# Kernel optimization log

Measured on AMD Instinct MI355X. Metric: run time of the kernel, lower is better.

## Reference

```python
import jax, jax.numpy as jnp
import numpy as np

D_MODEL = 1024
N_HEADS = 16
D_FF = 4096
EPS = 1e-5


def _layer_norm(x, scale, bias):
    mu = jnp.mean(x, axis=-1, keepdims=True)
    var = jnp.mean(jnp.square(x - mu), axis=-1, keepdims=True)
    return (x - mu) * jax.lax.rsqrt(var + EPS) * scale + bias


def setup_inputs() -> dict:
    key = jax.random.key(0)
    ks = jax.random.split(key, 12)
    B, L, D, F = 8, 1024, D_MODEL, D_FF
    s = 0.02
    inp = {
        "x": jax.random.normal(ks[0], (B, L, D), dtype=jnp.float32),
        "mask": jax.random.randint(ks[1], (B, L, L), 0, 2).astype(bool),
        "Wq": jax.random.normal(ks[2], (D, D), dtype=jnp.float32) * s,
        "bq": jnp.zeros((D,), jnp.float32),
        "Wk": jax.random.normal(ks[3], (D, D), dtype=jnp.float32) * s,
        "bk": jnp.zeros((D,), jnp.float32),
        "Wv": jax.random.normal(ks[4], (D, D), dtype=jnp.float32) * s,
        "bv": jnp.zeros((D,), jnp.float32),
        "Wo": jax.random.normal(ks[5], (D, D), dtype=jnp.float32) * s,
        "bo": jnp.zeros((D,), jnp.float32),
        "ln1_s": jnp.ones((D,), jnp.float32),
        "ln1_b": jnp.zeros((D,), jnp.float32),
        "ln2_s": jnp.ones((D,), jnp.float32),
        "ln2_b": jnp.zeros((D,), jnp.float32),
        "W1": jax.random.normal(ks[6], (F, D), dtype=jnp.float32) * s,
        "b1": jnp.zeros((F,), jnp.float32),
        "W2": jax.random.normal(ks[7], (D, F), dtype=jnp.float32) * s,
        "b2": jnp.zeros((D,), jnp.float32),
    }
    return inp


def _block(x, mask, Wq, bq, Wk, bk, Wv, bv, Wo, bo,
           ln1_s, ln1_b, ln2_s, ln2_b, W1, b1, W2, b2):
    B, L, D = x.shape
    H = N_HEADS
    dk = D // H
    xn = _layer_norm(x, ln1_s, ln1_b)
    # torch Linear: y = x @ W.T + b
    Q = (xn @ Wq.T + bq).reshape(B, L, H, dk).transpose(0, 2, 1, 3)  # [B,H,L,dk]
    K = (xn @ Wk.T + bk).reshape(B, L, H, dk).transpose(0, 2, 1, 3)
    V = (xn @ Wv.T + bv).reshape(B, L, H, dk).transpose(0, 2, 1, 3)
    scores = jnp.einsum('bhqd,bhkd->bhqk', Q, K) / jnp.sqrt(jnp.float32(dk))
    m = mask[:, None, :, :]                                    # [B,1,Lq,Lk]
    scores = jnp.where(m, -jnp.inf, scores)
    fully_masked = jnp.all(m, axis=-1, keepdims=True)          # [B,1,Lq,1]
    scores = jnp.where(fully_masked, 0.0, scores)
    attn = jax.nn.softmax(scores, axis=-1)
    attn = jnp.where(fully_masked, 0.0, attn)
    out = jnp.einsum('bhqk,bhkd->bhqd', attn, V)               # [B,H,L,dk]
    out = out.transpose(0, 2, 1, 3).reshape(B, L, D)
    attn_out = out @ Wo.T + bo
    x = x + attn_out
    xn2 = _layer_norm(x, ln2_s, ln2_b)
    h = jax.nn.gelu(xn2 @ W1.T + b1, approximate=False)        # exact GELU (torch default)
    ff = h @ W2.T + b2
    return x + ff


def reference(x, mask, Wq, bq, Wk, bk, Wv, bv, Wo, bo,
              ln1_s, ln1_b, ln2_s, ln2_b, W1, b1, W2, b2):
    return _block(x, mask, Wq, bq, Wk, bk, Wv, bv, Wo, bo,
                  ln1_s, ln1_b, ln2_s, ln2_b, W1, b1, W2, b2)
```

## Files before the change

### kernel.cpp

```cpp
#include <hip/hip_runtime.h>
#include <cstdint>
#include <cstddef>

typedef __attribute__((ext_vector_type(8))) short short8;
typedef __attribute__((ext_vector_type(4))) float f32x4;
typedef __attribute__((ext_vector_type(4))) unsigned short ushort4v;

#define DEVI __device__ __forceinline__

DEVI unsigned short f2bf(float f) {
  union { float f; unsigned u; } x; x.f = f;
  unsigned r = x.u + 0x7fffu + ((x.u >> 16) & 1u);
  return (unsigned short)(r >> 16);
}

#define MFMA16(a, b, c) __builtin_amdgcn_mfma_f32_16x16x32_bf16(a, b, c, 0, 0, 0)
#define FENCE asm volatile("" ::: "memory")
#define WAITVM(n) asm volatile("s_waitcnt vmcnt(" #n ")" ::: "memory")
#define WAITLGKM0 asm volatile("s_waitcnt lgkmcnt(0)" ::: "memory")
#define BARRIER do { FENCE; __builtin_amdgcn_s_barrier(); FENCE; } while (0)

typedef __attribute__((address_space(1))) const void g_void;
typedef __attribute__((address_space(3))) void lds_void;
DEVI void gload_lds16(const void* g, void* l) {
  __builtin_amdgcn_global_load_lds((g_void*)g, (lds_void*)l, 16, 0, 0);
}

static constexpr int DM = 1024;
static constexpr int NH = 16;
static constexpr int DK = 64;
static constexpr int FF = 4096;
static constexpr int BB = 8;
static constexpr int LL = 1024;
static constexpr int TT = BB * LL;

__global__ __launch_bounds__(256) void prep_kernel(
    const float* __restrict__ Wq, const float* __restrict__ Wk,
    const float* __restrict__ Wv, const float* __restrict__ Wo,
    const float* __restrict__ W1, const float* __restrict__ W2,
    const float* __restrict__ bq, const float* __restrict__ bk,
    const float* __restrict__ bv,
    unsigned short* __restrict__ wqkv, unsigned short* __restrict__ wob,
    unsigned short* __restrict__ w1b, unsigned short* __restrict__ w2b,
    float* __restrict__ bqkv, const unsigned* __restrict__ mask,
    int* __restrict__ flag) {
  int b = blockIdx.x;
  if (b < 6144) {
    int i = b * 256 + threadIdx.x;
    const float* src; unsigned short* dst; int li;
    if (i < 131072)      { src = Wq; dst = wqkv;             li = i; }
    else if (i < 262144) { src = Wk; dst = wqkv + (1 << 20); li = i - 131072; }
    else if (i < 393216) { src = Wv; dst = wqkv + (2 << 20); li = i - 262144; }
    else if (i < 524288) { src = Wo; dst = wob;              li = i - 393216; }
    else if (i < 1048576){ src = W1; dst = w1b;              li = i - 524288; }
    else                 { src = W2; dst = w2b;              li = i - 1048576; }
    const f32x4* s4 = (const f32x4*)src;
    f32x4 a = s4[li * 2], c = s4[li * 2 + 1];
    short8 o;
    o[0] = (short)f2bf(a[0]); o[1] = (short)f2bf(a[1]);
    o[2] = (short)f2bf(a[2]); o[3] = (short)f2bf(a[3]);
    o[4] = (short)f2bf(c[0]); o[5] = (short)f2bf(c[1]);
    o[6] = (short)f2bf(c[2]); o[7] = (short)f2bf(c[3]);
    *(short8*)(dst + (size_t)li * 8) = o;
  } else if (b < 6156) {
    int i = (b - 6144) * 256 + threadIdx.x;
    bqkv[i] = (i < 1024) ? bq[i] : (i < 2048 ? bk[i - 1024] : bv[i - 2048]);
  } else {
    unsigned a = 0;
    for (int i = threadIdx.x; i < 4096; i += 256) a |= mask[i];
    #pragma unroll
    for (int off = 32; off >= 1; off >>= 1) a |= __shfl_xor(a, off);
    __shared__ unsigned sh[4];
    if ((threadIdx.x & 63) == 0) sh[threadIdx.x >> 6] = a;
    __syncthreads();
    if (threadIdx.x == 0) {
      unsigned o = sh[0] | sh[1] | sh[2] | sh[3];
      flag[0] = (o & 0xFEFEFEFEu) ? 2 : ((o & 0xFFFFFF00u) ? 1 : 0);
    }
  }
}

__global__ __launch_bounds__(256) void ln_kernel(const float* __restrict__ x,
                                                 const float* __restrict__ sc,
                                                 const float* __restrict__ bi,
                                                 unsigned short* __restrict__ out,
                                                 const void* __restrict__ mask,
                                                 unsigned* __restrict__ mp,
                                                 const int* __restrict__ flag,
                                                 int npack) {
  int row = blockIdx.x;
  int t = threadIdx.x;
  if (row >= TT) {
    int w = (row - TT) * 256 + t;
    int cls = flag[0];
    unsigned bits = 0u;
    if (cls == 1) {
      const unsigned char* mb = (const unsigned char*)mask + (size_t)w * 32;
      #pragma unroll 8
      for (int i = 0; i < 32; ++i) bits |= (mb[i] ? 1u : 0u) << i;
    } else {
      const unsigned* mi = (const unsigned*)mask + (size_t)w * 32;
      #pragma unroll 8
      for (int i = 0; i < 32; ++i) bits |= (mi[i] ? 1u : 0u) << i;
    }
    mp[w] = bits;
    return;
  }
  const f32x4* xr = (const f32x4*)(x + (size_t)row * DM);
  f32x4 v = xr[t];
  float s = v[0] + v[1] + v[2] + v[3];
  float q = v[0]*v[0] + v[1]*v[1] + v[2]*v[2] + v[3]*v[3];
  #pragma unroll
  for (int off = 32; off >= 1; off >>= 1) { s += __shfl_xor(s, off); q += __shfl_xor(q, off); }
  __shared__ float red[8];
  int wv = t >> 6;
  if ((t & 63) == 0) { red[wv] = s; red[4 + wv] = q; }
  __syncthreads();
  s = red[0] + red[1] + red[2] + red[3];
  q = red[4] + red[5] + red[6] + red[7];
  float mu = s * (1.0f / DM);
  float var = q * (1.0f / DM) - mu * mu;
  float rs = rsqrtf(var + 1e-5f);
  f32x4 sv = ((const f32x4*)sc)[t], bv = ((const f32x4*)bi)[t];
  ushort4v o;
  #pragma unroll
  for (int j = 0; j < 4; ++j) o[j] = f2bf((v[j] - mu) * rs * sv[j] + bv[j]);
  *(ushort4v*)(out + (size_t)row * DM + t * 4) = o;
}

template <int EPI>
__global__ __launch_bounds__(256, 2)
void gemm5(const unsigned short* __restrict__ A, const unsigned short* __restrict__ Bw,
           const float* __restrict__ bias, void* __restrict__ out0,
           void* __restrict__ out1, void* __restrict__ out2,
           const float* __restrict__ res, int N, int K) {
  __shared__ __align__(16) char smem[65536];
  const int t = threadIdx.x;
  const int w = t >> 6, ln = t & 63;
  const int wm = w >> 1, wn = w & 1;
  const int lg = ln >> 4, lc = ln & 15;
  const int m0 = blockIdx.x * 128, n0 = blockIdx.y * 128;
  const size_t rb = (size_t)K * 2;
  const int nk = K >> 6;

  const char* srcp[8];
  #pragma unroll
  for (int i = 0; i < 8; ++i) {
    int off = i * 4096 + t * 16;
    if (off < 16384) {
      int r = off >> 7, c = (off >> 4) & 7;
      srcp[i] = (const char*)A + (size_t)(m0 + r) * rb + ((c ^ (r & 7)) << 4);
    } else {
      int ob = off - 16384;
      int r = ob >> 7, c = (ob >> 4) & 7;
      srcp[i] = (const char*)Bw + (size_t)(n0 + r) * rb + ((c ^ (r & 7)) << 4);
    }
  }
  auto stage8 = [&](int tile) {
    char* db = smem + ((tile & 1) << 15) + t * 16;
    const size_t ko = (size_t)tile << 7;
    #pragma unroll
    for (int i = 0; i < 8; ++i) gload_lds16(srcp[i] + ko, db + i * 4096);
  };

  int aoff[4][2], boff[4][2];
  #pragma unroll
  for (int x_ = 0; x_ < 4; ++x_)
    #pragma unroll
    for (int kk = 0; kk < 2; ++kk) {
      int ra = wm * 64 + x_ * 16 + lc;
      aoff[x_][kk] = ra * 128 + (((kk * 4 + lg) ^ (ra & 7)) << 4);
      int rn = wn * 64 + x_ * 16 + lc;
      boff[x_][kk] = 16384 + rn * 128 + (((kk * 4 + lg) ^ (rn & 7)) << 4);
    }

  f32x4 acc[4][4] = {};

  stage8(0);
  for (int T = 0; T < nk; ++T) {
    if (T + 1 < nk) stage8(T + 1);
    if (T == nk - 1) { WAITVM(0); } else { WAITVM(8); }
    BARRIER;
    const char* buf = smem + ((T & 1) << 15);
    short8 afr[4][2], bfr[4][2];
    #pragma unroll
    for (int ni = 0; ni < 4; ++ni) {
      bfr[ni][0] = *(const short8*)(buf + boff[ni][0]);
      bfr[ni][1] = *(const short8*)(buf + boff[ni][1]);
    }
    #pragma unroll
    for (int mi = 0; mi < 4; ++mi) {
      afr[mi][0] = *(const short8*)(buf + aoff[mi][0]);
      afr[mi][1] = *(const short8*)(buf + aoff[mi][1]);
    }
    __builtin_amdgcn_s_setprio(1);
    #pragma unroll
    for (int mi = 0; mi < 4; ++mi)
      #pragma unroll
      for (int ni = 0; ni < 4; ++ni) {
        acc[mi][ni] = MFMA16(afr[mi][0], bfr[ni][0], acc[mi][ni]);
        acc[mi][ni] = MFMA16(afr[mi][1], bfr[ni][1], acc[mi][ni]);
      }
    __builtin_amdgcn_s_setprio(0);
    WAITLGKM0;
    BARRIER;
  }
  __syncthreads();

  const int colb = n0 + wn * 64 + lc;
  const int rowb = m0 + wm * 64 + lg * 4;
  if constexpr (EPI >= 2) {
    #pragma unroll
    for (int ni = 0; ni < 4; ++ni) {
      int col = colb + ni * 16;
      float bv = bias[col];
      #pragma unroll
      for (int mi = 0; mi < 4; ++mi)
        #pragma unroll
        for (int rr = 0; rr < 4; ++rr) {
          int row = rowb + mi * 16 + rr;
          float v = acc[mi][ni][rr] + bv;
          if constexpr (EPI == 2)
            ((float*)out0)[(size_t)row * N + col] = res[(size_t)row * N + col] + v;
          else
            ((float*)out0)[(size_t)row * N + col] += v;
        }
    }
  } else {
    short* sl = (short*)(smem + w * 9216);
    const bool isV = (EPI == 0) && (n0 + wn * 64 >= 2048);
    #pragma unroll
    for (int ni = 0; ni < 4; ++ni) {
      float bv = bias[colb + ni * 16];
      #pragma unroll
      for (int mi = 0; mi < 4; ++mi)
        #pragma unroll
        for (int rr = 0; rr < 4; ++rr) {
          int row_l = mi * 16 + lg * 4 + rr;
          int col_l = ni * 16 + lc;
          float v = acc[mi][ni][rr] + bv;
          if constexpr (EPI == 1) {
            float u2 = v * v;
            float mexp = v * (-2.302206744f - 0.102953795f * u2);
            v = v / (1.0f + exp2f(mexp));
          }
          if (isV) sl[col_l * 72 + row_l] = (short)f2bf(v);
          else     sl[row_l * 72 + col_l] = (short)f2bf(v);
        }
    }
    const int s8 = ln >> 3, c8 = ln & 7;
    if constexpr (EPI == 0) {
      const int b_ = m0 >> 10;
      const int l0 = (m0 & 1023) + wm * 64;
      const int h_ = ((n0 + wn * 64) >> 6) & 15;
      const size_t bh = (size_t)(b_ * NH + h_);
      if (n0 + wn * 64 < 2048) {
        char* dst = (char*)((n0 + wn * 64 < 1024) ? out0 : out1) + (((bh << 10) + l0) << 7);
        #pragma unroll
        for (int j = 0; j < 8; ++j) {
          short8 v8 = *(const short8*)(sl + (j * 8 + s8) * 72 + c8 * 8);
          *(short8*)(dst + j * 1024 + ln * 16) = v8;
        }
      } else {
        char* dst = (char*)out2 + bh * 131072 + l0 * 2 + c8 * 16;
        #pragma unroll
        for (int j = 0; j < 8; ++j) {
          short8 v8 = *(const short8*)(sl + (j * 8 + s8) * 72 + c8 * 8);
          *(short8*)(dst + (size_t)(j * 8 + s8) * 2048) = v8;
        }
      }
    } else {
      char* dst = (char*)out0 + (size_t)(m0 + wm * 64) * ((size_t)N * 2) +
                  (size_t)(n0 + wn * 64) * 2 + c8 * 16;
      #pragma unroll
      for (int j = 0; j < 8; ++j) {
        short8 v8 = *(const short8*)(sl + (j * 8 + s8) * 72 + c8 * 8);
        *(short8*)(dst + (size_t)(j * 8 + s8) * ((size_t)N * 2)) = v8;
      }
    }
  }
}

__global__ __launch_bounds__(512) void attn_kernel(const unsigned short* __restrict__ Q,
                                                   const unsigned short* __restrict__ Kb,
                                                   const unsigned short* __restrict__ Vt,
                                                   const unsigned* __restrict__ mp,
                                                   unsigned short* __restrict__ ctx) {
  __shared__ __align__(16) char kv[2][16384];
  __shared__ __align__(16) short plds[8][16][72];
  const int t = threadIdx.x, wv = t >> 6, ln = t & 63;
  const int bid = blockIdx.x;
  const int wg = (bid & 7) * 128 + (bid >> 3);
  const int qt = wg & 7, h_ = (wg >> 3) & 15, b_ = wg >> 7;
  const int bh = b_ * NH + h_;
  const int lg = ln >> 4, lc = ln & 15;
  const int qrow0 = qt * 128 + wv * 16;

  const unsigned short* qbase = Q + ((size_t)bh * LL + qrow0) * DK;
  short8 qf0 = *(const short8*)(qbase + (size_t)lc * DK + lg * 8);
  short8 qf1 = *(const short8*)(qbase + (size_t)lc * DK + 32 + lg * 8);

  short8 onesf;
  #pragma unroll
  for (int j = 0; j < 8; ++j) onesf[j] = (short)0x3F80;

  f32x4 o[4] = {};
  f32x4 o_l = {};

  const char* kg = (const char*)(Kb + (size_t)bh * LL * DK);
  const char* vg = (const char*)(Vt + (size_t)bh * DK * LL);
  const int srow = ln >> 3;
  const int gc = (ln & 7) ^ srow;
  const char* ksrc = kg + (size_t)(wv * 8 + srow) * 128 + gc * 16;
  const char* vsrc = vg + (size_t)(wv * 8 + srow) * 2048 + gc * 16;

  const unsigned* mrow = mp + ((size_t)b_ * LL + qrow0) * 32;

  gload_lds16(ksrc, kv[0] + wv * 1024);
  gload_lds16(vsrc, kv[0] + 8192 + wv * 1024);
  __syncthreads();

  int cur = 0;
  for (int kt = 0; kt < 16; ++kt) {
    if (kt < 15) {
      gload_lds16(ksrc + (size_t)(kt + 1) * 8192, kv[cur ^ 1] + wv * 1024);
      gload_lds16(vsrc + (size_t)(kt + 1) * 128, kv[cur ^ 1] + 8192 + wv * 1024);
    }
    const char* kb_ = kv[cur];
    const char* vb_ = kv[cur] + 8192;
    f32x4 s[4] = {};
    #pragma unroll
    for (int c = 0; c < 4; ++c) {
      int row = c * 16 + lc;
      short8 k0 = *(const short8*)(kb_ + row * 128 + ((lg) ^ (row & 7)) * 16);
      short8 k1 = *(const short8*)(kb_ + row * 128 + ((4 + lg) ^ (row & 7)) * 16);
      s[c] = MFMA16(qf0, k0, s[c]);
      s[c] = MFMA16(qf1, k1, s[c]);
    }
    unsigned wrd[4][2];
    #pragma unroll
    for (int r = 0; r < 4; ++r) {
      const unsigned* mr = mrow + (size_t)(lg * 4 + r) * 32 + kt * 2;
      wrd[r][0] = mr[0]; wrd[r][1] = mr[1];
    }
    #pragma unroll
    for (int c = 0; c < 4; ++c)
      #pragma unroll
      for (int r = 0; r < 4; ++r) {
        bool mk = (wrd[r][c >> 1] >> ((c & 1) * 16 + lc)) & 1;
        float p = mk ? 0.0f : exp2f(fmaf(s[c][r], 0.18033688011112f, -16.0f));
        plds[wv][lg * 4 + r][c * 16 + lc] = (short)f2bf(p);
      }
    #pragma unroll
    for (int kk = 0; kk < 2; ++kk) {
      short8 pf = *(const short8*)&plds[wv][lc][kk * 32 + lg * 8];
      o_l = MFMA16(pf, onesf, o_l);
      #pragma unroll
      for (int dt = 0; dt < 4; ++dt) {
        int row = dt * 16 + lc;
        short8 vf = *(const short8*)(vb_ + row * 128 + ((kk * 4 + lg) ^ (row & 7)) * 16);
        o[dt] = MFMA16(pf, vf, o[dt]);
      }
    }
    __syncthreads();
    cur ^= 1;
  }
  #pragma unroll
  for (int r = 0; r < 4; ++r) {
    float l = o_l[r];
    float inv = (l > 0.0f) ? 1.0f / l : 0.0f;
    size_t trow = (size_t)b_ * LL + qt * 128 + wv * 16 + lg * 4 + r;
    #pragma unroll
    for (int dt = 0; dt < 4; ++dt)
      ctx[trow * DM + h_ * 64 + dt * 16 + lc] = f2bf(o[dt][r] * inv);
  }
}

extern "C" void kernel_launch(void* const* d_in, const int* in_sizes, int n_in,
                              void* d_out, int out_size, void* d_ws, size_t ws_size,
                              hipStream_t stream) {
  const float* x   = (const float*)d_in[0];
  const void*  msk = d_in[1];
  const float* Wq = (const float*)d_in[2],  *bq = (const float*)d_in[3];
  const float* Wk = (const float*)d_in[4],  *bk = (const float*)d_in[5];
  const float* Wv = (const float*)d_in[6],  *bv = (const float*)d_in[7];
  const float* Wo = (const float*)d_in[8],  *bo = (const float*)d_in[9];
  const float* l1s = (const float*)d_in[10], *l1b = (const float*)d_in[11];
  const float* l2s = (const float*)d_in[12], *l2b = (const float*)d_in[13];
  const float* W1 = (const float*)d_in[14], *b1 = (const float*)d_in[15];
  const float* W2 = (const float*)d_in[16], *b2 = (const float*)d_in[17];
  float* out = (float*)d_out;
  char* ws = (char*)d_ws;
  const size_t MB = 1u << 20;

  unsigned short* wqkv = (unsigned short*)(ws + 0 * MB);
  unsigned short* wob = (unsigned short*)(ws + 6 * MB);
  unsigned short* w1b = (unsigned short*)(ws + 8 * MB);
  unsigned short* w2b = (unsigned short*)(ws + 16 * MB);
  unsigned short* xn  = (unsigned short*)(ws + 24 * MB);
  unsigned short* qb  = (unsigned short*)(ws + 40 * MB);
  unsigned short* kb  = (unsigned short*)(ws + 56 * MB);
  unsigned short* vtb = (unsigned short*)(ws + 72 * MB);
  unsigned*       mpk = (unsigned*)(ws + 88 * MB);
  float*          bqkv = (float*)(ws + 89 * MB);
  int*            flg = (int*)(ws + 89 * MB + 65536);
  unsigned short* ctx = xn;
  unsigned short* xn2 = qb;
  unsigned short* hb  = (unsigned short*)(ws + 90 * MB);

  int mchunk;
  size_t avail = (ws_size > 90 * MB) ? ws_size - 90 * MB : 0;
  if      (avail >= 64 * MB) mchunk = 8192;
  else if (avail >= 16 * MB) mchunk = 2048;
  else if (avail >= 4 * MB)  mchunk = 512;
  else                       mchunk = 256;

  prep_kernel<<<6157, 256, 0, stream>>>(Wq, Wk, Wv, Wo, W1, W2, bq, bk, bv,
                                        wqkv, wob, w1b, w2b, bqkv,
                                        (const unsigned*)msk, flg);

  ln_kernel<<<TT + 1024, 256, 0, stream>>>(x, l1s, l1b, xn, msk, mpk, flg, 1024);

  gemm5<0><<<dim3(64, 24), 256, 0, stream>>>(xn, wqkv, bqkv, qb, kb, vtb,
                                             nullptr, 3072, DM);

  attn_kernel<<<1024, 512, 0, stream>>>(qb, kb, vtb, mpk, ctx);

  gemm5<2><<<dim3(64, 8), 256, 0, stream>>>(ctx, wob, bo, out, nullptr, nullptr,
                                            x, DM, DM);

  ln_kernel<<<TT, 256, 0, stream>>>(out, l2s, l2b, xn2, nullptr, nullptr, flg, 0);

  for (int off = 0; off < TT; off += mchunk) {
    gemm5<1><<<dim3(mchunk / 128, 32), 256, 0, stream>>>(
        xn2 + (size_t)off * DM, w1b, b1, hb, nullptr, nullptr, nullptr, FF, DM);
    gemm5<3><<<dim3(mchunk / 128, 8), 256, 0, stream>>>(
        hb, w2b, b2, out + (size_t)off * DM, nullptr, nullptr, nullptr, DM, FF);
  }
}
```

Baseline: 387.9 us.

## Add 256x256-tile 8-wave GEMM with split-phase pipeline for QKV and FFN1

```diff
diff --git a/kernel.cpp b/kernel.cpp
--- a/kernel.cpp
+++ b/kernel.cpp
@@ -281,6 +281,193 @@
   }
 }
 
+template <int EPI>
+__global__ __launch_bounds__(512, 2)
+void gemm8(const unsigned short* __restrict__ A, const unsigned short* __restrict__ Bw,
+           const float* __restrict__ bias, void* __restrict__ out0,
+           void* __restrict__ out1, void* __restrict__ out2, int N, int K) {
+  __shared__ __align__(16) char smem[131072];
+  const int t = threadIdx.x;
+  const int w = t >> 6, ln = t & 63;
+  const int wm = w >> 2, wn = w & 3;
+  const int lg = ln >> 4, lc = ln & 15;
+
+  const int gx = gridDim.x;
+  const int nwg = gx * gridDim.y;
+  int bid = blockIdx.y * gx + blockIdx.x;
+  if ((nwg & 7) == 0) bid = (bid & 7) * (nwg >> 3) + (bid >> 3);
+  const int m0 = (bid % gx) * 256, n0 = (bid / gx) * 256;
+
+  const int nk = K >> 6;
+
+  int srcA[4], srcB[4];
+  #pragma unroll
+  for (int i = 0; i < 4; ++i) {
+    int off = i * 8192 + t * 16;
+    int r = off >> 7, c = (off >> 4) & 7;
+    int sw = (c ^ (r & 7)) << 4;
+    srcA[i] = (m0 + r) * (K * 2) + sw;
+    srcB[i] = (n0 + r) * (K * 2) + sw;
+  }
+  auto stage_half = [&](int tile, int h) {
+    char* db = smem + ((tile & 1) << 16) + (h << 14) + t * 16;
+    const int ko = tile << 7;
+    if (h < 2) {
+      gload_lds16((const char*)A + srcA[2 * h] + ko, db);
+      gload_lds16((const char*)A + srcA[2 * h + 1] + ko, db + 8192);
+    } else {
+      gload_lds16((const char*)Bw + srcB[2 * h - 4] + ko, db);
+      gload_lds16((const char*)Bw + srcB[2 * h - 3] + ko, db + 8192);
+    }
+  };
+
+  f32x4 acc[8][4] = {};
+  const int arow = wm * 128 + lc;
+  const int brow = wn * 64 + lc;
+
+  stage_half(0, 0); stage_half(0, 1); stage_half(0, 2); stage_half(0, 3);
+  stage_half(1, 0); stage_half(1, 1); stage_half(1, 2);
+  WAITVM(6);
+  BARRIER;
+
+  for (int T = 0; T < nk; ++T) {
+    const char* bufA = smem + ((T & 1) << 16);
+    const char* bufB = bufA + 32768;
+    short8 a0[4][2], a1[4][2], b[2][2];
+    #pragma unroll
+    for (int mi = 0; mi < 4; ++mi) {
+      int ra = arow + mi * 16, sw = ra & 7;
+      a0[mi][0] = *(const short8*)(bufA + ra * 128 + ((lg ^ sw) << 4));
+      a0[mi][1] = *(const short8*)(bufA + ra * 128 + (((4 + lg) ^ sw) << 4));
+    }
+    #pragma unroll
+    for (int ni = 0; ni < 2; ++ni) {
+      int rn = brow + ni * 16, sw = rn & 7;
+      b[ni][0] = *(const short8*)(bufB + rn * 128 + ((lg ^ sw) << 4));
+      b[ni][1] = *(const short8*)(bufB + rn * 128 + (((4 + lg) ^ sw) << 4));
+    }
+    if (T + 1 < nk) stage_half(T + 1, 3);
+    BARRIER; WAITLGKM0;
+    __builtin_amdgcn_s_setprio(1);
+    #pragma unroll
+    for (int mi = 0; mi < 4; ++mi)
+      #pragma unroll
+      for (int ni = 0; ni < 2; ++ni) {
+        acc[mi][ni] = MFMA16(a0[mi][0], b[ni][0], acc[mi][ni]);
+        acc[mi][ni] = MFMA16(a0[mi][1], b[ni][1], acc[mi][ni]);
+      }
+    __builtin_amdgcn_s_setprio(0);
+    BARRIER;
+    #pragma unroll
+    for (int mi = 0; mi < 4; ++mi) {
+      int ra = arow + 64 + mi * 16, sw = ra & 7;
+      a1[mi][0] = *(const short8*)(bufA + ra * 128 + ((lg ^ sw) << 4));
+      a1[mi][1] = *(const short8*)(bufA + ra * 128 + (((4 + lg) ^ sw) << 4));
+    }
+    BARRIER; WAITLGKM0;
+    __builtin_amdgcn_s_setprio(1);
+    #pragma unroll
+    for (int mi = 0; mi < 4; ++mi)
+      #pragma unroll
+      for (int ni = 0; ni < 2; ++ni) {
+        acc[4 + mi][ni] = MFMA16(a1[mi][0], b[ni][0], acc[4 + mi][ni]);
+        acc[4 + mi][ni] = MFMA16(a1[mi][1], b[ni][1], acc[4 + mi][ni]);
+      }
+    __builtin_amdgcn_s_setprio(0);
+    BARRIER;
+    #pragma unroll
+    for (int ni = 0; ni < 2; ++ni) {
+      int rn = brow + 32 + ni * 16, sw = rn & 7;
+      b[ni][0] = *(const short8*)(bufB + rn * 128 + ((lg ^ sw) << 4));
+      b[ni][1] = *(const short8*)(bufB + rn * 128 + (((4 + lg) ^ sw) << 4));
+    }
+    if (T + 2 < nk) stage_half(T + 2, 0);
+    BARRIER; WAITLGKM0;
+    __builtin_amdgcn_s_setprio(1);
+    #pragma unroll
+    for (int mi = 0; mi < 4; ++mi)
+      #pragma unroll
+      for (int ni = 0; ni < 2; ++ni) {
+        acc[mi][2 + ni] = MFMA16(a0[mi][0], b[ni][0], acc[mi][2 + ni]);
+        acc[mi][2 + ni] = MFMA16(a0[mi][1], b[ni][1], acc[mi][2 + ni]);
+      }
+    __builtin_amdgcn_s_setprio(0);
+    BARRIER;
+    if (T + 2 < nk) { stage_half(T + 2, 1); stage_half(T + 2, 2); }
+    BARRIER;
+    __builtin_amdgcn_s_setprio(1);
+    #pragma unroll
+    for (int mi = 0; mi < 4; ++mi)
+      #pragma unroll
+      for (int ni = 0; ni < 2; ++ni) {
+        acc[4 + mi][2 + ni] = MFMA16(a1[mi][0], b[ni][0], acc[4 + mi][2 + ni]);
+        acc[4 + mi][2 + ni] = MFMA16(a1[mi][1], b[ni][1], acc[4 + mi][2 + ni]);
+      }
+    __builtin_amdgcn_s_setprio(0);
+    if (T < nk - 2) { WAITVM(6); } else if (T == nk - 2) { WAITVM(0); }
+    BARRIER;
+  }
+  __syncthreads();
+
+  const int colb = n0 + wn * 64 + lc;
+  short* sl = (short*)(smem + w * 9216);
+  const int s8 = ln >> 3, c8 = ln & 7;
+  const bool isV = (EPI == 0) && (n0 + wn * 64 >= 2048);
+  #pragma unroll
+  for (int p = 0; p < 2; ++p) {
+    if (p) { WAITLGKM0; }
+    #pragma unroll
+    for (int ni = 0; ni < 4; ++ni) {
+      float bv = bias[colb + ni * 16];
+      #pragma unroll
+      for (int mi = 0; mi < 4; ++mi)
+        #pragma unroll
+        for (int rr = 0; rr < 4; ++rr) {
+          int row_l = mi * 16 + lg * 4 + rr;
+          int col_l = ni * 16 + lc;
+          float v = acc[p * 4 + mi][ni][rr] + bv;
+          if constexpr (EPI == 1) {
+            float u2 = v * v;
+            float mexp = v * (-2.302206744f - 0.102953795f * u2);
+            v = v / (1.0f + exp2f(mexp));
+          }
+          if (isV) sl[col_l * 72 + row_l] = (short)f2bf(v);
+          else     sl[row_l * 72 + col_l] = (short)f2bf(v);
+        }
+    }
+    if constexpr (EPI == 0) {
+      const int b_ = m0 >> 10;
+      const int l0 = (m0 & 1023) + wm * 128 + p * 64;
+      const int h_ = ((n0 + wn * 64) >> 6) & 15;
+      const size_t bh = (size_t)(b_ * NH + h_);
+      if (!isV) {
+        char* dst = (char*)((n0 + wn * 64 < 1024) ? out0 : out1) +
+                    (((bh << 10) + (size_t)l0) << 7);
+        #pragma unroll
+        for (int j = 0; j < 8; ++j) {
+          short8 v8 = *(const short8*)(sl + (j * 8 + s8) * 72 + c8 * 8);
+          *(short8*)(dst + j * 1024 + ln * 16) = v8;
+        }
+      } else {
+        char* dst = (char*)out2 + bh * 131072 + (size_t)l0 * 2 + c8 * 16;
+        #pragma unroll
+        for (int j = 0; j < 8; ++j) {
+          short8 v8 = *(const short8*)(sl + (j * 8 + s8) * 72 + c8 * 8);
+          *(short8*)(dst + (size_t)(j * 8 + s8) * 2048) = v8;
+        }
+      }
+    } else {
+      char* dst = (char*)out0 + (size_t)(m0 + wm * 128 + p * 64) * ((size_t)N * 2) +
+                  (size_t)(n0 + wn * 64) * 2 + c8 * 16;
+      #pragma unroll
+      for (int j = 0; j < 8; ++j) {
+        short8 v8 = *(const short8*)(sl + (j * 8 + s8) * 72 + c8 * 8);
+        *(short8*)(dst + (size_t)(j * 8 + s8) * ((size_t)N * 2)) = v8;
+      }
+    }
+  }
+}
+
 __global__ __launch_bounds__(512) void attn_kernel(const unsigned short* __restrict__ Q,
                                                    const unsigned short* __restrict__ Kb,
                                                    const unsigned short* __restrict__ Vt,
@@ -421,8 +608,8 @@
 
   ln_kernel<<<TT + 1024, 256, 0, stream>>>(x, l1s, l1b, xn, msk, mpk, flg, 1024);
 
-  gemm5<0><<<dim3(64, 24), 256, 0, stream>>>(xn, wqkv, bqkv, qb, kb, vtb,
-                                             nullptr, 3072, DM);
+  gemm8<0><<<dim3(32, 12), 512, 0, stream>>>(xn, wqkv, bqkv, qb, kb, vtb,
+                                             3072, DM);
 
   attn_kernel<<<1024, 512, 0, stream>>>(qb, kb, vtb, mpk, ctx);
 
@@ -432,8 +619,8 @@
   ln_kernel<<<TT, 256, 0, stream>>>(out, l2s, l2b, xn2, nullptr, nullptr, flg, 0);
 
   for (int off = 0; off < TT; off += mchunk) {
-    gemm5<1><<<dim3(mchunk / 128, 32), 256, 0, stream>>>(
-        xn2 + (size_t)off * DM, w1b, b1, hb, nullptr, nullptr, nullptr, FF, DM);
+    gemm8<1><<<dim3(mchunk / 256, 16), 512, 0, stream>>>(
+        xn2 + (size_t)off * DM, w1b, b1, hb, nullptr, nullptr, FF, DM);
     gemm5<3><<<dim3(mchunk / 128, 8), 256, 0, stream>>>(
         hb, w2b, b2, out + (size_t)off * DM, nullptr, nullptr, nullptr, DM, FF);
   }
```

Result: slower. 396.6 us (+2.2%).
